# Performance work log

Hardware: AMD Instinct MI355X
Metric: run time of the kernel (lower is better)

## Reference

```python
import jax, jax.numpy as jnp
import numpy as np

C, D, B = 32768, 1024, 16384
LABEL = 0.95  # EMA keep factor from __init__ default


def setup_inputs() -> dict:
    key = jax.random.key(0)
    k1, k2, k3, k4 = jax.random.split(key, 4)
    return {
        "s_logits": jax.random.normal(k1, (C, D), dtype=jnp.float32),
        "t_logits": jax.random.normal(k2, (C, D), dtype=jnp.float32),
        "logits": jax.random.normal(k3, (B, D), dtype=jnp.float32),
        "the_class": jax.random.randint(k4, (B,), 0, C, dtype=jnp.int64),
    }


def _ema_scatter(table, logits, the_class, keep):
    """Sequential per-row EMA: for i in range(B): table[c_i] = table[c_i]*keep + logits[i]*(1-keep).
    Vectorized: row c with k occurrences -> table[c]*keep^k + (1-keep)*sum_j keep^{#later occurrences} * logits[j].
    """
    Bn = the_class.shape[0]
    Cn = table.shape[0]
    dt = table.dtype
    ones = jnp.ones((Bn,), dtype=dt)
    counts = jax.ops.segment_sum(ones, the_class, num_segments=Cn)  # [C]
    # occurrence rank (0-based, in original batch order) of each sample within its class
    order = jnp.argsort(the_class)  # stable sort preserves batch order within a class
    sc = the_class[order]
    first = jnp.searchsorted(sc, sc, side="left")  # start of each class segment
    rank_sorted = jnp.arange(Bn, dtype=jnp.int32) - first.astype(jnp.int32)
    rank = jnp.zeros((Bn,), jnp.int32).at[order].set(rank_sorted)
    # number of later same-class occurrences
    r = counts[the_class] - 1.0 - rank.astype(dt)  # [B]
    w = (1.0 - keep) * jnp.power(jnp.asarray(keep, dt), r)  # [B]
    contrib = jax.ops.segment_sum(logits * w[:, None], the_class, num_segments=Cn)  # [C, D]
    decay = jnp.power(jnp.asarray(keep, dt), counts)  # [C]; rows absent from batch keep decay=1
    return table * decay[:, None] + contrib


def reference(s_logits, t_logits, logits, the_class):
    new_s = _ema_scatter(s_logits, logits, the_class, LABEL)  # update(type='s')
    loss = jnp.mean(jnp.sum(jnp.abs(new_s - t_logits), axis=1))  # loss()
    return loss
```

## Files before the change

### kernel.cpp

```cpp
#include <hip/hip_runtime.h>

#define NC 32768
#define ND 1024
#define NB 16384
#define KEEP 0.95f
#define OMK  0.05f
#define KCAP 16

__global__ void count_scatter_kernel(const int* __restrict__ the_class,
                                     int* __restrict__ counts,
                                     int* __restrict__ class_list) {
    int i = blockIdx.x * blockDim.x + threadIdx.x;
    if (i < NB) {
        int c = the_class[i];
        int pos = atomicAdd(&counts[c], 1);
        if (pos < KCAP) class_list[c * KCAP + pos] = i;
    }
}

__global__ __launch_bounds__(256) void loss_kernel(
    const float* __restrict__ s_logits,
    const float* __restrict__ t_logits,
    const float* __restrict__ logits,
    const int*   __restrict__ counts,
    const int*   __restrict__ class_list,
    float* __restrict__ out) {

    const int wave = threadIdx.x >> 6;
    const int lane = threadIdx.x & 63;
    const int c = blockIdx.x * 4 + wave;

    const int cnt = counts[c];

    float decay;
    {
        float base = KEEP, r = 1.0f;
        int e = cnt;
        while (e > 0) { if (e & 1) r *= base; base *= base; e >>= 1; }
        decay = r;
    }

    const int m = cnt < KCAP ? cnt : KCAP;

    int myidx = 0x7fffffff;
    if (lane < m) myidx = class_list[c * KCAP + lane];
    int r_later = 0;
    for (int l = 0; l < m; ++l) {
        int other = __shfl(myidx, l);
        if (other > myidx) r_later++;
    }
    float myw = OMK;
    for (int k = 0; k < r_later; ++k) myw *= KEEP;

    const float4* s4 = (const float4*)(s_logits + (size_t)c * ND);
    const float4* t4 = (const float4*)(t_logits + (size_t)c * ND);

    float lsum = 0.0f;
    #pragma unroll
    for (int k = 0; k < 4; ++k) {
        const int q = lane + k * 64;
        float4 sv = s4[q];
        float4 acc;
        acc.x = sv.x * decay;
        acc.y = sv.y * decay;
        acc.z = sv.z * decay;
        acc.w = sv.w * decay;
        for (int j = 0; j < m; ++j) {
            const int   ij = __shfl(myidx, j);
            const float wj = __shfl(myw, j);
            const float4* l4 = (const float4*)(logits + (size_t)ij * ND);
            float4 lv = l4[q];
            acc.x += wj * lv.x;
            acc.y += wj * lv.y;
            acc.z += wj * lv.z;
            acc.w += wj * lv.w;
        }
        float4 tv = t4[q];
        lsum += fabsf(acc.x - tv.x) + fabsf(acc.y - tv.y) +
                fabsf(acc.z - tv.z) + fabsf(acc.w - tv.w);
    }

    #pragma unroll
    for (int off = 32; off > 0; off >>= 1) lsum += __shfl_down(lsum, off);

    __shared__ float wsum[4];
    if (lane == 0) wsum[wave] = lsum;
    __syncthreads();
    if (threadIdx.x == 0) {
        float total = (wsum[0] + wsum[1] + wsum[2] + wsum[3]) * (1.0f / NC);
        atomicAdd(out, total);
    }
}

extern "C" void kernel_launch(void* const* d_in, const int* in_sizes, int n_in,
                              void* d_out, int out_size, void* d_ws, size_t ws_size,
                              hipStream_t stream) {
    const float* s_logits  = (const float*)d_in[0];
    const float* t_logits  = (const float*)d_in[1];
    const float* logits    = (const float*)d_in[2];
    const int*   the_class = (const int*)d_in[3];
    float* out = (float*)d_out;

    int* counts     = (int*)d_ws;
    int* class_list = counts + NC;

    hipMemsetAsync(counts, 0, NC * sizeof(int), stream);
    hipMemsetAsync(d_out, 0, sizeof(float), stream);

    count_scatter_kernel<<<NB / 256, 256, 0, stream>>>(the_class, counts, class_list);
    loss_kernel<<<NC / 4, 256, 0, stream>>>(s_logits, t_logits, logits,
                                            counts, class_list, out);
}
```

Before: 351.7 us.

## Precompute per-class weights in prep kernel and batch 8 rows per block

Adds a small prep kernel that computes each class's decay factor and its (sample index, EMA weight) list, so the main kernel no longer does per-wave rank and weight computation with shuffles. The loss kernel now has each thread own one float4 column across 8 consecutive class rows and issues all s and t loads up front, which raises memory-level parallelism. This costs an extra kernel launch, extra workspace traffic, and more registers per thread. The per-row loop over contributing samples now loads each weight entry from global memory instead of reading it through a shuffle.

```diff
diff --git a/kernel.cpp b/kernel.cpp
--- a/kernel.cpp
+++ b/kernel.cpp
@@ -2,19 +2,43 @@
 
 #define NC 32768
 #define ND 1024
+#define NQ 256
 #define NB 16384
 #define KEEP 0.95f
 #define OMK  0.05f
 #define KCAP 16
+#define RPB 8
 
 __global__ void count_scatter_kernel(const int* __restrict__ the_class,
                                      int* __restrict__ counts,
-                                     int* __restrict__ class_list) {
+                                     int* __restrict__ idx_list) {
     int i = blockIdx.x * blockDim.x + threadIdx.x;
     if (i < NB) {
         int c = the_class[i];
         int pos = atomicAdd(&counts[c], 1);
-        if (pos < KCAP) class_list[c * KCAP + pos] = i;
+        if (pos < KCAP) idx_list[c * KCAP + pos] = i;
+    }
+}
+
+__global__ void wprep_kernel(const int* __restrict__ counts,
+                             const int* __restrict__ idx_list,
+                             float* __restrict__ decays,
+                             int2* __restrict__ elist) {
+    int c = blockIdx.x * blockDim.x + threadIdx.x;
+    int cnt = counts[c];
+    float base = KEEP, r = 1.0f;
+    for (int e = cnt; e > 0; e >>= 1) { if (e & 1) r *= base; base *= base; }
+    decays[c] = r;
+    int m = cnt < KCAP ? cnt : KCAP;
+    int idx[KCAP];
+    for (int j = 0; j < m; ++j) idx[j] = idx_list[c * KCAP + j];
+    for (int j = 0; j < m; ++j) {
+        int later = 0;
+        for (int l = 0; l < m; ++l) later += (idx[l] > idx[j]);
+        float w = OMK;
+        for (int k = 0; k < later; ++k) w *= KEEP;
+        int2 e; e.x = idx[j]; e.y = __float_as_int(w);
+        elist[c * KCAP + j] = e;
     }
 }
 
@@ -23,67 +47,57 @@
     const float* __restrict__ t_logits,
     const float* __restrict__ logits,
     const int*   __restrict__ counts,
-    const int*   __restrict__ class_list,
+    const float* __restrict__ decays,
+    const int2*  __restrict__ elist,
     float* __restrict__ out) {
 
-    const int wave = threadIdx.x >> 6;
-    const int lane = threadIdx.x & 63;
-    const int c = blockIdx.x * 4 + wave;
+    const int q  = threadIdx.x;
+    const int c0 = blockIdx.x * RPB;
 
-    const int cnt = counts[c];
+    const float4* s4 = (const float4*)s_logits;
+    const float4* t4 = (const float4*)t_logits;
+    const float4* l4 = (const float4*)logits;
 
-    float decay;
-    {
-        float base = KEEP, r = 1.0f;
-        int e = cnt;
-        while (e > 0) { if (e & 1) r *= base; base *= base; e >>= 1; }
-        decay = r;
+    float4 sv[RPB], tv[RPB];
+    #pragma unroll
+    for (int r = 0; r < RPB; ++r) sv[r] = s4[(size_t)(c0 + r) * NQ + q];
+    #pragma unroll
+    for (int r = 0; r < RPB; ++r) tv[r] = t4[(size_t)(c0 + r) * NQ + q];
+
+    float dec[RPB]; int m[RPB];
+    #pragma unroll
+    for (int r = 0; r < RPB; ++r) {
+        dec[r] = decays[c0 + r];
+        int cnt = counts[c0 + r];
+        m[r] = cnt < KCAP ? cnt : KCAP;
     }
-
-    const int m = cnt < KCAP ? cnt : KCAP;
-
-    int myidx = 0x7fffffff;
-    if (lane < m) myidx = class_list[c * KCAP + lane];
-    int r_later = 0;
-    for (int l = 0; l < m; ++l) {
-        int other = __shfl(myidx, l);
-        if (other > myidx) r_later++;
-    }
-    float myw = OMK;
-    for (int k = 0; k < r_later; ++k) myw *= KEEP;
-
-    const float4* s4 = (const float4*)(s_logits + (size_t)c * ND);
-    const float4* t4 = (const float4*)(t_logits + (size_t)c * ND);
 
     float lsum = 0.0f;
     #pragma unroll
-    for (int k = 0; k < 4; ++k) {
-        const int q = lane + k * 64;
-        float4 sv = s4[q];
+    for (int r = 0; r < RPB; ++r) {
+        const int c = c0 + r;
         float4 acc;
-        acc.x = sv.x * decay;
-        acc.y = sv.y * decay;
-        acc.z = sv.z * decay;
-        acc.w = sv.w * decay;
-        for (int j = 0; j < m; ++j) {
-            const int   ij = __shfl(myidx, j);
-            const float wj = __shfl(myw, j);
-            const float4* l4 = (const float4*)(logits + (size_t)ij * ND);
-            float4 lv = l4[q];
-            acc.x += wj * lv.x;
-            acc.y += wj * lv.y;
-            acc.z += wj * lv.z;
-            acc.w += wj * lv.w;
+        acc.x = sv[r].x * dec[r];
+        acc.y = sv[r].y * dec[r];
+        acc.z = sv[r].z * dec[r];
+        acc.w = sv[r].w * dec[r];
+        for (int j = 0; j < m[r]; ++j) {
+            int2 e = elist[c * KCAP + j];
+            const float w = __int_as_float(e.y);
+            float4 lv = l4[(size_t)e.x * NQ + q];
+            acc.x = fmaf(w, lv.x, acc.x);
+            acc.y = fmaf(w, lv.y, acc.y);
+            acc.z = fmaf(w, lv.z, acc.z);
+            acc.w = fmaf(w, lv.w, acc.w);
         }
-        float4 tv = t4[q];
-        lsum += fabsf(acc.x - tv.x) + fabsf(acc.y - tv.y) +
-                fabsf(acc.z - tv.z) + fabsf(acc.w - tv.w);
+        lsum += fabsf(acc.x - tv[r].x) + fabsf(acc.y - tv[r].y) +
+                fabsf(acc.z - tv[r].z) + fabsf(acc.w - tv[r].w);
     }
 
     #pragma unroll
     for (int off = 32; off > 0; off >>= 1) lsum += __shfl_down(lsum, off);
-
     __shared__ float wsum[4];
+    const int wave = threadIdx.x >> 6, lane = threadIdx.x & 63;
     if (lane == 0) wsum[wave] = lsum;
     __syncthreads();
     if (threadIdx.x == 0) {
@@ -101,13 +115,16 @@
     const int*   the_class = (const int*)d_in[3];
     float* out = (float*)d_out;
 
-    int* counts     = (int*)d_ws;
-    int* class_list = counts + NC;
+    int*   counts   = (int*)d_ws;
+    int*   idx_list = counts + NC;
+    float* decays   = (float*)(idx_list + NC * KCAP);
+    int2*  elist    = (int2*)(decays + NC);
 
     hipMemsetAsync(counts, 0, NC * sizeof(int), stream);
     hipMemsetAsync(d_out, 0, sizeof(float), stream);
 
-    count_scatter_kernel<<<NB / 256, 256, 0, stream>>>(the_class, counts, class_list);
-    loss_kernel<<<NC / 4, 256, 0, stream>>>(s_logits, t_logits, logits,
-                                            counts, class_list, out);
+    count_scatter_kernel<<<NB / 256, 256, 0, stream>>>(the_class, counts, idx_list);
+    wprep_kernel<<<NC / 256, 256, 0, stream>>>(counts, idx_list, decays, elist);
+    loss_kernel<<<NC / RPB, 256, 0, stream>>>(s_logits, t_logits, logits,
+                                              counts, decays, elist, out);
 }
```

Measured after the change: 335.9 us. 1.05x faster.
